# Performance work log

Hardware: AMD Instinct MI355X
Metric: run time of the kernel (lower is better)

## Reference

```python
import jax, jax.numpy as jnp
import numpy as np

B, N, M = 16, 4096, 4096

def setup_inputs() -> dict:
    key = jax.random.key(0)
    k1, k2, k3 = jax.random.split(key, 3)
    src_points = jax.random.normal(k1, (B, N, 3), dtype=jnp.float32)
    tgt_points = jax.random.normal(k2, (B, M, 3), dtype=jnp.float32)
    weights = jax.random.uniform(k3, (B,), dtype=jnp.float32)
    return {"src_points": src_points, "tgt_points": tgt_points, "weights": weights}

def reference(src_points, tgt_points, weights):
    # Pairwise squared distances per batch: [B, N, M]
    # ||s - t||^2 = ||s||^2 + ||t||^2 - 2 s.t  (single dense intermediate)
    s2 = jnp.sum(src_points * src_points, axis=-1)  # [B, N]
    t2 = jnp.sum(tgt_points * tgt_points, axis=-1)  # [B, M]
    cross = jnp.einsum('bnd,bmd->bnm', src_points, tgt_points)  # [B, N, M]
    d2 = s2[:, :, None] + t2[:, None, :] - 2.0 * cross          # [B, N, M]
    d2 = jnp.maximum(d2, 0.0)  # numerical guard
    # Bidirectional chamfer: mean of nearest-neighbor squared distances
    d_src_to_tgt = jnp.mean(jnp.min(d2, axis=2), axis=1)  # [B]
    d_tgt_to_src = jnp.mean(jnp.min(d2, axis=1), axis=1)  # [B]
    distances = d_src_to_tgt + d_tgt_to_src               # [B]
    distances = distances * weights
    return jnp.mean(distances)  # reduction='mean'
```

## Files before the change

kernel.cpp:

```cpp
#include <hip/hip_runtime.h>

#define BQ 16
#define NP 4096
#define MP 4096

constexpr int TPB = 256;
constexpr int SRC_PER_THREAD = 8;
constexpr int NCHUNK = TPB * SRC_PER_THREAD;
constexpr int MSPLIT = 16;
constexpr int MSLICE = MP / MSPLIT;
constexpr int TILE = 256;

__global__ void chamfer_init_kernel(unsigned int* __restrict__ minbuf, int n,
                                    float* __restrict__ out) {
    int i = blockIdx.x * blockDim.x + threadIdx.x;
    if (i < n) minbuf[i] = 0x7F800000u;
    if (i == 0) out[0] = 0.0f;
}

__global__ __launch_bounds__(TPB) void chamfer_dir_kernel(
    const float* __restrict__ srcp,
    const float* __restrict__ tgtp,
    unsigned int* __restrict__ minbuf
) {
    const int bz  = blockIdx.z;
    const int dir = (bz >= BQ) ? 1 : 0;
    const int b   = dir ? (bz - BQ) : bz;

    const float* S = dir ? (tgtp + (size_t)b * MP * 3) : (srcp + (size_t)b * NP * 3);
    const float* T = dir ? (srcp + (size_t)b * NP * 3) : (tgtp + (size_t)b * MP * 3);
    unsigned int* outmin = minbuf + ((size_t)dir * BQ + b) * NP;

    __shared__ float4 tile[TILE];

    {
        const int m = blockIdx.y * MSLICE + threadIdx.x;
        const float* p = T + (size_t)m * 3;
        float tx = p[0], ty = p[1], tz = p[2];
        float t2 = fmaf(tx, tx, fmaf(ty, ty, tz * tz));
        tile[threadIdx.x] = make_float4(-2.0f * tx, -2.0f * ty, -2.0f * tz, t2);
    }

    const int nbase = blockIdx.x * NCHUNK + threadIdx.x;
    float sx[SRC_PER_THREAD], sy[SRC_PER_THREAD], sz[SRC_PER_THREAD];
#pragma unroll
    for (int k = 0; k < SRC_PER_THREAD; ++k) {
        const float* p = S + (size_t)(nbase + k * TPB) * 3;
        sx[k] = p[0];
        sy[k] = p[1];
        sz[k] = p[2];
    }

    float mn[SRC_PER_THREAD];
#pragma unroll
    for (int k = 0; k < SRC_PER_THREAD; ++k) mn[k] = __int_as_float(0x7F800000);

    __syncthreads();

#pragma unroll 2
    for (int j = 0; j < TILE; j += 2) {
        float4 ta = tile[j];
        float4 tb = tile[j + 1];
#pragma unroll
        for (int k = 0; k < SRC_PER_THREAD; ++k) {
            float v1 = fmaf(sx[k], ta.x, fmaf(sy[k], ta.y, fmaf(sz[k], ta.z, ta.w)));
            float v2 = fmaf(sx[k], tb.x, fmaf(sy[k], tb.y, fmaf(sz[k], tb.z, tb.w)));
            mn[k] = fminf(mn[k], fminf(v1, v2));
        }
    }

#pragma unroll
    for (int k = 0; k < SRC_PER_THREAD; ++k) {
        float s2 = fmaf(sx[k], sx[k], fmaf(sy[k], sy[k], sz[k] * sz[k]));
        float d  = fmaxf(mn[k] + s2, 0.0f);
        atomicMin(&outmin[nbase + k * TPB], __float_as_uint(d));
    }
}

__global__ __launch_bounds__(TPB) void chamfer_reduce_kernel(
    const float* __restrict__ minbuf,
    const float* __restrict__ weights,
    float* __restrict__ out) {
    const int idx = blockIdx.x;
    const int b = idx & (BQ - 1);
    const float* m0 = minbuf + (size_t)idx * NP;

    float s = 0.0f;
    for (int i = threadIdx.x; i < NP; i += TPB) s += m0[i];

#pragma unroll
    for (int off = 32; off > 0; off >>= 1) s += __shfl_down(s, off, 64);

    __shared__ float red[TPB / 64];
    if ((threadIdx.x & 63) == 0) red[threadIdx.x >> 6] = s;
    __syncthreads();
    if (threadIdx.x == 0) {
        float tot = 0.0f;
#pragma unroll
        for (int w = 0; w < TPB / 64; ++w) tot += red[w];
        atomicAdd(out, weights[b] * tot * (1.0f / ((float)NP * (float)BQ)));
    }
}

extern "C" void kernel_launch(void* const* d_in, const int* in_sizes, int n_in,
                              void* d_out, int out_size, void* d_ws, size_t ws_size,
                              hipStream_t stream) {
    const float* src = (const float*)d_in[0];
    const float* tgt = (const float*)d_in[1];
    const float* wts = (const float*)d_in[2];
    float* out = (float*)d_out;

    unsigned int* minbuf = (unsigned int*)d_ws;
    const int minElems = 2 * BQ * NP;

    chamfer_init_kernel<<<(minElems + TPB - 1) / TPB, TPB, 0, stream>>>(
        minbuf, minElems, out);

    dim3 grid(NP / NCHUNK, MSPLIT, 2 * BQ);
    chamfer_dir_kernel<<<grid, TPB, 0, stream>>>(src, tgt, minbuf);

    chamfer_reduce_kernel<<<2 * BQ, TPB, 0, stream>>>((const float*)minbuf, wts, out);
}
```

Before: 105.3 us.

## Compute chamfer distances with bf16 split-precision MFMA and fuse reduction

Replaces the scalar FMA distance loop with 32x32x16 bf16 MFMA instructions. Coordinates and squared norms are split into hi/lo bf16 pairs so the matrix product reproduces s2 + t2 - 2 s.t at near-fp32 accuracy. Each block now owns a set of source points and scans all targets, so the per-point atomicMin buffer, the init kernel and the separate reduce kernel are removed and the weighted mean is accumulated directly. The cost is extra conversion work per target chunk, two barriers per chunk, and some loss of precision from the bf16 splitting.

```diff
diff --git a/kernel.cpp b/kernel.cpp
--- a/kernel.cpp
+++ b/kernel.cpp
@@ -5,100 +5,126 @@
 #define MP 4096
 
 constexpr int TPB = 256;
-constexpr int SRC_PER_THREAD = 8;
-constexpr int NCHUNK = TPB * SRC_PER_THREAD;
-constexpr int MSPLIT = 16;
-constexpr int MSLICE = MP / MSPLIT;
-constexpr int TILE = 256;
+constexpr int CHUNK = 256;
+constexpr int SRC_PER_BLOCK = 128;
 
-__global__ void chamfer_init_kernel(unsigned int* __restrict__ minbuf, int n,
-                                    float* __restrict__ out) {
-    int i = blockIdx.x * blockDim.x + threadIdx.x;
-    if (i < n) minbuf[i] = 0x7F800000u;
-    if (i == 0) out[0] = 0.0f;
+typedef __bf16 bf16x8 __attribute__((ext_vector_type(8)));
+typedef float f32x16 __attribute__((ext_vector_type(16)));
+
+union Frag {
+    unsigned short u[8];
+    bf16x8 v;
+    int4 i4;
+};
+
+__device__ inline unsigned short f2bf(float f) {
+    unsigned u = __float_as_uint(f);
+    return (unsigned short)((u + 0x7FFFu + ((u >> 16) & 1u)) >> 16);
+}
+__device__ inline float bf2f(unsigned short h) {
+    return __uint_as_float(((unsigned)h) << 16);
 }
 
-__global__ __launch_bounds__(TPB) void chamfer_dir_kernel(
+__global__ void chamfer_zero_kernel(float* __restrict__ out) { out[0] = 0.0f; }
+
+__global__ __launch_bounds__(TPB) void chamfer_mfma_kernel(
     const float* __restrict__ srcp,
     const float* __restrict__ tgtp,
-    unsigned int* __restrict__ minbuf
-) {
-    const int bz  = blockIdx.z;
-    const int dir = (bz >= BQ) ? 1 : 0;
-    const int b   = dir ? (bz - BQ) : bz;
-
+    const float* __restrict__ wts,
+    float* __restrict__ out)
+{
+    const int gy  = blockIdx.y;
+    const int dir = gy >> 4;
+    const int b   = gy & 15;
     const float* S = dir ? (tgtp + (size_t)b * MP * 3) : (srcp + (size_t)b * NP * 3);
     const float* T = dir ? (srcp + (size_t)b * NP * 3) : (tgtp + (size_t)b * MP * 3);
-    unsigned int* outmin = minbuf + ((size_t)dir * BQ + b) * NP;
 
-    __shared__ float4 tile[TILE];
+    const int tid  = threadIdx.x;
+    const int lane = tid & 63;
+    const int half = lane >> 5;
+    const int col  = lane & 31;
+    const int wave = tid >> 6;
 
+    __shared__ unsigned short sh[CHUNK * 16];
+    __shared__ float partial[TPB / 64];
+
+    const unsigned short ONE = 0x3F80;
+
+    Frag bfrag;
     {
-        const int m = blockIdx.y * MSLICE + threadIdx.x;
-        const float* p = T + (size_t)m * 3;
-        float tx = p[0], ty = p[1], tz = p[2];
-        float t2 = fmaf(tx, tx, fmaf(ty, ty, tz * tz));
-        tile[threadIdx.x] = make_float4(-2.0f * tx, -2.0f * ty, -2.0f * tz, t2);
-    }
-
-    const int nbase = blockIdx.x * NCHUNK + threadIdx.x;
-    float sx[SRC_PER_THREAD], sy[SRC_PER_THREAD], sz[SRC_PER_THREAD];
-#pragma unroll
-    for (int k = 0; k < SRC_PER_THREAD; ++k) {
-        const float* p = S + (size_t)(nbase + k * TPB) * 3;
-        sx[k] = p[0];
-        sy[k] = p[1];
-        sz[k] = p[2];
-    }
-
-    float mn[SRC_PER_THREAD];
-#pragma unroll
-    for (int k = 0; k < SRC_PER_THREAD; ++k) mn[k] = __int_as_float(0x7F800000);
-
-    __syncthreads();
-
-#pragma unroll 2
-    for (int j = 0; j < TILE; j += 2) {
-        float4 ta = tile[j];
-        float4 tb = tile[j + 1];
-#pragma unroll
-        for (int k = 0; k < SRC_PER_THREAD; ++k) {
-            float v1 = fmaf(sx[k], ta.x, fmaf(sy[k], ta.y, fmaf(sz[k], ta.z, ta.w)));
-            float v2 = fmaf(sx[k], tb.x, fmaf(sy[k], tb.y, fmaf(sz[k], tb.z, tb.w)));
-            mn[k] = fminf(mn[k], fminf(v1, v2));
+        const int sidx = blockIdx.x * SRC_PER_BLOCK + wave * 32 + col;
+        const float* sp = S + (size_t)sidx * 3;
+        float x = sp[0], y = sp[1], z = sp[2];
+        unsigned short uh0 = f2bf(-2.0f * x), uh1 = f2bf(-2.0f * y), uh2 = f2bf(-2.0f * z);
+        unsigned short ul0 = f2bf(-2.0f * x - bf2f(uh0));
+        unsigned short ul1 = f2bf(-2.0f * y - bf2f(uh1));
+        unsigned short ul2 = f2bf(-2.0f * z - bf2f(uh2));
+        float s2 = fmaf(x, x, fmaf(y, y, z * z));
+        unsigned short s2h = f2bf(s2), s2l = f2bf(s2 - bf2f(s2h));
+        if (half == 0) {
+            bfrag.u[0] = uh0; bfrag.u[1] = uh1; bfrag.u[2] = uh2;
+            bfrag.u[3] = ul0; bfrag.u[4] = ul1; bfrag.u[5] = ul2;
+            bfrag.u[6] = uh0; bfrag.u[7] = uh1;
+        } else {
+            bfrag.u[0] = uh2; bfrag.u[1] = ONE; bfrag.u[2] = ONE;
+            bfrag.u[3] = s2h; bfrag.u[4] = s2l;
+            bfrag.u[5] = 0;   bfrag.u[6] = 0;   bfrag.u[7] = 0;
         }
     }
 
-#pragma unroll
-    for (int k = 0; k < SRC_PER_THREAD; ++k) {
-        float s2 = fmaf(sx[k], sx[k], fmaf(sy[k], sy[k], sz[k] * sz[k]));
-        float d  = fmaxf(mn[k] + s2, 0.0f);
-        atomicMin(&outmin[nbase + k * TPB], __float_as_uint(d));
-    }
-}
+    float accm = __int_as_float(0x7F800000);
 
-__global__ __launch_bounds__(TPB) void chamfer_reduce_kernel(
-    const float* __restrict__ minbuf,
-    const float* __restrict__ weights,
-    float* __restrict__ out) {
-    const int idx = blockIdx.x;
-    const int b = idx & (BQ - 1);
-    const float* m0 = minbuf + (size_t)idx * NP;
-
-    float s = 0.0f;
-    for (int i = threadIdx.x; i < NP; i += TPB) s += m0[i];
+    for (int c = 0; c < MP / CHUNK; ++c) {
+        {
+            const float* tp = T + (size_t)(c * CHUNK + tid) * 3;
+            float x = tp[0], y = tp[1], z = tp[2];
+            unsigned short xh = f2bf(x), yh = f2bf(y), zh = f2bf(z);
+            unsigned short xl = f2bf(x - bf2f(xh));
+            unsigned short yl = f2bf(y - bf2f(yh));
+            unsigned short zl = f2bf(z - bf2f(zh));
+            float t2 = fmaf(x, x, fmaf(y, y, z * z));
+            unsigned short t2h = f2bf(t2), t2l = f2bf(t2 - bf2f(t2h));
+            Frag p0, p1;
+            p0.u[0] = xh; p0.u[1] = yh; p0.u[2] = zh;
+            p0.u[3] = xh; p0.u[4] = yh; p0.u[5] = zh;
+            p0.u[6] = xl; p0.u[7] = yl;
+            p1.u[0] = zl;
+            p1.u[1] = t2h; p1.u[2] = t2l;
+            p1.u[3] = ONE; p1.u[4] = ONE;
+            p1.u[5] = 0; p1.u[6] = 0; p1.u[7] = 0;
+            const int sub = tid >> 5, row = tid & 31;
+            *(int4*)&sh[sub * 512 + row * 8]       = p0.i4;
+            *(int4*)&sh[sub * 512 + 256 + row * 8] = p1.i4;
+        }
+        __syncthreads();
 
 #pragma unroll
-    for (int off = 32; off > 0; off >>= 1) s += __shfl_down(s, off, 64);
+        for (int sc = 0; sc < CHUNK / 32; ++sc) {
+            Frag a;
+            a.i4 = *(const int4*)&sh[sc * 512 + half * 256 + col * 8];
+            f32x16 zc = {};
+            f32x16 d = __builtin_amdgcn_mfma_f32_32x32x16_bf16(a.v, bfrag.v, zc, 0, 0, 0);
+            float m0 = fminf(fminf(d[0], d[1]), d[2]);
+            float m1 = fminf(fminf(d[3], d[4]), d[5]);
+            float m2 = fminf(fminf(d[6], d[7]), d[8]);
+            float m3 = fminf(fminf(d[9], d[10]), d[11]);
+            float m4 = fminf(fminf(d[12], d[13]), d[14]);
+            float t0 = fminf(fminf(m0, m1), m2);
+            float t1 = fminf(fminf(m3, m4), d[15]);
+            accm = fminf(fminf(accm, t0), t1);
+        }
+        __syncthreads();
+    }
 
-    __shared__ float red[TPB / 64];
-    if ((threadIdx.x & 63) == 0) red[threadIdx.x >> 6] = s;
+    float m = fminf(accm, __shfl_xor(accm, 32, 64));
+    m = fmaxf(m, 0.0f);
+#pragma unroll
+    for (int off = 16; off > 0; off >>= 1) m += __shfl_xor(m, off, 64);
+    if (lane == 0) partial[wave] = m;
     __syncthreads();
-    if (threadIdx.x == 0) {
-        float tot = 0.0f;
-#pragma unroll
-        for (int w = 0; w < TPB / 64; ++w) tot += red[w];
-        atomicAdd(out, weights[b] * tot * (1.0f / ((float)NP * (float)BQ)));
+    if (tid == 0) {
+        float v = partial[0] + partial[1] + partial[2] + partial[3];
+        atomicAdd(out, v * wts[b] * (1.0f / ((float)NP * (float)BQ)));
     }
 }
 
@@ -110,14 +136,8 @@
     const float* wts = (const float*)d_in[2];
     float* out = (float*)d_out;
 
-    unsigned int* minbuf = (unsigned int*)d_ws;
-    const int minElems = 2 * BQ * NP;
+    chamfer_zero_kernel<<<1, 1, 0, stream>>>(out);
 
-    chamfer_init_kernel<<<(minElems + TPB - 1) / TPB, TPB, 0, stream>>>(
-        minbuf, minElems, out);
-
-    dim3 grid(NP / NCHUNK, MSPLIT, 2 * BQ);
-    chamfer_dir_kernel<<<grid, TPB, 0, stream>>>(src, tgt, minbuf);
-
-    chamfer_reduce_kernel<<<2 * BQ, TPB, 0, stream>>>((const float*)minbuf, wts, out);
+    dim3 grid(NP / SRC_PER_BLOCK, 2 * BQ);
+    chamfer_mfma_kernel<<<grid, TPB, 0, stream>>>(src, tgt, wts, out);
 }
```

New measurement: 91.55 us. 13.1% less time.
